# Kernel optimization log

Measured on AMD Instinct MI355X. Metric: run time of the kernel, lower is better.

Reference implementation:

```python
import jax, jax.numpy as jnp
import numpy as np


def setup_inputs() -> dict:
    key = jax.random.key(0)
    k1, k2, k3, k4 = jax.random.split(key, 4)
    B, C, Cr, H, W = 4, 32, 16, 64, 128
    return {
        "left_img": jax.random.normal(k1, (B, C, H, W), dtype=jnp.float32),
        "reduce_left_img": jax.random.normal(k2, (B, Cr, H, W), dtype=jnp.float32),
        "right_img": jax.random.normal(k3, (B, C, H, W), dtype=jnp.float32),
        "reduce_right_img": jax.random.normal(k4, (B, Cr, H, W), dtype=jnp.float32),
        "max_disp": 48,
    }


def reference(left_img, reduce_left_img, right_img, reduce_right_img, max_disp):
    # left_img, right_img: [B, C, H, W]; reduce_*: [B, Cr, H, W]
    B, C, H, W = left_img.shape
    D = int(max_disp)
    d = jnp.arange(D)
    cols = jnp.arange(W)
    # valid columns j >= disparity i, zero elsewhere (matches zero_() buffers)
    mask = (cols[None, :] >= d[:, None]).astype(left_img.dtype)  # [D, W]
    mask5 = mask[:, None, :]                                     # [D, 1, W] -> bcast [B,Ch,D,H,W]
    src = jnp.clip(cols[None, :] - d[:, None], 0, W - 1)         # [D, W] shifted source cols

    def shift(x):
        # x: [B, Ch, H, W] -> right-shifted by d with zero fill: [B, Ch, D, H, W]
        y = x[:, :, :, src]              # [B, Ch, H, D, W]
        return jnp.moveaxis(y, 3, 2) * mask5

    l = left_img[:, :, None, :, :] * mask5   # [B, C, D, H, W]
    r = shift(right_img)                     # [B, C, D, H, W]
    ave = (l + r) / 2
    ave2 = (l * l + r * r) / 2
    cost_var = ave2 - ave * ave              # = ((l-r)/2)^2, zero where masked

    cat_l = reduce_left_img[:, :, None, :, :] * mask5  # [B, Cr, D, H, W]
    cat_r = shift(reduce_right_img)                    # [B, Cr, D, H, W]

    # torch: cat((cost_var, cost_cat), 1) with cost_cat = [left_half, right_half]
    return jnp.concatenate([cost_var, cat_l, cat_r], axis=1)
```

## Files before the change

### kernel.cpp

```cpp
#include <hip/hip_runtime.h>

typedef unsigned int u32;
typedef float f32x4 __attribute__((ext_vector_type(4)));

__global__ __launch_bounds__(256) void costvol_kernel(
    const float* __restrict__ left, const float* __restrict__ rleft,
    const float* __restrict__ right, const float* __restrict__ rright,
    float* __restrict__ out)
{
    const u32 bid = blockIdx.x;
    const u32 h = bid & 63u;
    const u32 t = bid >> 6;
    const u32 c = t & 63u;
    const u32 b = t >> 6;
    const u32 tid = threadIdx.x;

    __shared__ float rrow[132];

    const u32 w0 = (tid & 31u) * 4u;
    const u32 d0 = tid >> 5;
    float* orow = out + (size_t)((b * 64u + c) * 48u) * 8192u
                      + (size_t)h * 128u + w0;

    if (c < 32u) {
        const u32 base = ((b * 32u + c) * 64u + h) * 128u;
        if (tid < 128u) rrow[tid + (tid >> 5)] = right[base + tid];
        __syncthreads();

        const float4 l = ((const float4*)(left + base))[tid & 31u];
        const float lv[4] = { l.x, l.y, l.z, l.w };

        #pragma unroll
        for (u32 it = 0; it < 6u; ++it) {
            const u32 d = it * 8u + d0;
            float o[4];
            #pragma unroll
            for (int j = 0; j < 4; ++j) {
                const u32 w = w0 + (u32)j;
                const bool act = (w >= d);
                const u32 idx = act ? (w - d) : 0u;
                const float r = rrow[idx + (idx >> 5)];
                const float tv = (lv[j] - r) * 0.5f;
                o[j] = act ? (tv * tv) : 0.0f;
            }
            f32x4 ov = { o[0], o[1], o[2], o[3] };
            __builtin_nontemporal_store(ov, (f32x4*)(orow + d * 8192u));
        }
    } else if (c < 48u) {
        const u32 base = ((b * 16u + (c - 32u)) * 64u + h) * 128u;
        const float4 v = ((const float4*)(rleft + base))[tid & 31u];

        #pragma unroll
        for (u32 it = 0; it < 6u; ++it) {
            const u32 d = it * 8u + d0;
            f32x4 ov = { (w0      >= d) ? v.x : 0.0f,
                         (w0 + 1u >= d) ? v.y : 0.0f,
                         (w0 + 2u >= d) ? v.z : 0.0f,
                         (w0 + 3u >= d) ? v.w : 0.0f };
            __builtin_nontemporal_store(ov, (f32x4*)(orow + d * 8192u));
        }
    } else {
        const u32 base = ((b * 16u + (c - 48u)) * 64u + h) * 128u;
        if (tid < 128u) rrow[tid + (tid >> 5)] = rright[base + tid];
        __syncthreads();

        #pragma unroll
        for (u32 it = 0; it < 6u; ++it) {
            const u32 d = it * 8u + d0;
            float o[4];
            #pragma unroll
            for (int j = 0; j < 4; ++j) {
                const u32 w = w0 + (u32)j;
                const bool act = (w >= d);
                const u32 idx = act ? (w - d) : 0u;
                o[j] = act ? rrow[idx + (idx >> 5)] : 0.0f;
            }
            f32x4 ov = { o[0], o[1], o[2], o[3] };
            __builtin_nontemporal_store(ov, (f32x4*)(orow + d * 8192u));
        }
    }
}

extern "C" void kernel_launch(void* const* d_in, const int* in_sizes, int n_in,
                              void* d_out, int out_size, void* d_ws, size_t ws_size,
                              hipStream_t stream) {
    const float* left   = (const float*)d_in[0];
    const float* rleft  = (const float*)d_in[1];
    const float* right  = (const float*)d_in[2];
    const float* rright = (const float*)d_in[3];
    float* out = (float*)d_out;
    const u32 blocks = 4u * 64u * 64u;
    costvol_kernel<<<blocks, 256, 0, stream>>>(left, rleft, right, rright, out);
}
```

Before: 393.8 us.

## Remap blocks to one output (b,c,d) plane with contiguous stores

```diff
diff --git a/kernel.cpp b/kernel.cpp
--- a/kernel.cpp
+++ b/kernel.cpp
@@ -9,74 +9,64 @@
     float* __restrict__ out)
 {
     const u32 bid = blockIdx.x;
-    const u32 h = bid & 63u;
-    const u32 t = bid >> 6;
+    const u32 d = bid % 48u;
+    const u32 t = bid / 48u;
     const u32 c = t & 63u;
     const u32 b = t >> 6;
     const u32 tid = threadIdx.x;
 
-    __shared__ float rrow[132];
-
-    const u32 w0 = (tid & 31u) * 4u;
-    const u32 d0 = tid >> 5;
-    float* orow = out + (size_t)((b * 64u + c) * 48u) * 8192u
-                      + (size_t)h * 128u + w0;
+    float* oplane = out + (size_t)bid * 8192u;
 
     if (c < 32u) {
-        const u32 base = ((b * 32u + c) * 64u + h) * 128u;
-        if (tid < 128u) rrow[tid + (tid >> 5)] = right[base + tid];
-        __syncthreads();
-
-        const float4 l = ((const float4*)(left + base))[tid & 31u];
-        const float lv[4] = { l.x, l.y, l.z, l.w };
-
+        const float* lp = left  + (size_t)(b * 32u + c) * 8192u;
+        const float* rp = right + (size_t)(b * 32u + c) * 8192u;
         #pragma unroll
-        for (u32 it = 0; it < 6u; ++it) {
-            const u32 d = it * 8u + d0;
+        for (u32 it = 0; it < 8u; ++it) {
+            const u32 flat = it * 1024u + tid * 4u;
+            const u32 w0 = flat & 127u;
+            const f32x4 l4 = *(const f32x4*)(lp + flat);
             float o[4];
             #pragma unroll
             for (int j = 0; j < 4; ++j) {
                 const u32 w = w0 + (u32)j;
                 const bool act = (w >= d);
-                const u32 idx = act ? (w - d) : 0u;
-                const float r = rrow[idx + (idx >> 5)];
-                const float tv = (lv[j] - r) * 0.5f;
+                const u32 ri = act ? (flat + (u32)j - d) : 0u;
+                const float r = rp[ri];
+                const float tv = (l4[j] - r) * 0.5f;
                 o[j] = act ? (tv * tv) : 0.0f;
             }
             f32x4 ov = { o[0], o[1], o[2], o[3] };
-            __builtin_nontemporal_store(ov, (f32x4*)(orow + d * 8192u));
+            __builtin_nontemporal_store(ov, (f32x4*)(oplane + flat));
         }
     } else if (c < 48u) {
-        const u32 base = ((b * 16u + (c - 32u)) * 64u + h) * 128u;
-        const float4 v = ((const float4*)(rleft + base))[tid & 31u];
-
+        const float* sp = rleft + (size_t)(b * 16u + (c - 32u)) * 8192u;
         #pragma unroll
-        for (u32 it = 0; it < 6u; ++it) {
-            const u32 d = it * 8u + d0;
-            f32x4 ov = { (w0      >= d) ? v.x : 0.0f,
-                         (w0 + 1u >= d) ? v.y : 0.0f,
-                         (w0 + 2u >= d) ? v.z : 0.0f,
-                         (w0 + 3u >= d) ? v.w : 0.0f };
-            __builtin_nontemporal_store(ov, (f32x4*)(orow + d * 8192u));
+        for (u32 it = 0; it < 8u; ++it) {
+            const u32 flat = it * 1024u + tid * 4u;
+            const u32 w0 = flat & 127u;
+            const f32x4 v = *(const f32x4*)(sp + flat);
+            f32x4 ov = { (w0      >= d) ? v[0] : 0.0f,
+                         (w0 + 1u >= d) ? v[1] : 0.0f,
+                         (w0 + 2u >= d) ? v[2] : 0.0f,
+                         (w0 + 3u >= d) ? v[3] : 0.0f };
+            __builtin_nontemporal_store(ov, (f32x4*)(oplane + flat));
         }
     } else {
-        const u32 base = ((b * 16u + (c - 48u)) * 64u + h) * 128u;
-        if (tid < 128u) rrow[tid + (tid >> 5)] = rright[base + tid];
-        __syncthreads();
-
+        const float* sp = rright + (size_t)(b * 16u + (c - 48u)) * 8192u;
         #pragma unroll
-        for (u32 it = 0; it < 6u; ++it) {
-            const u32 d = it * 8u + d0;
+        for (u32 it = 0; it < 8u; ++it) {
+            const u32 flat = it * 1024u + tid * 4u;
+            const u32 w0 = flat & 127u;
             float o[4];
             #pragma unroll
             for (int j = 0; j < 4; ++j) {
                 const u32 w = w0 + (u32)j;
                 const bool act = (w >= d);
-                const u32 idx = act ? (w - d) : 0u;
-                o[j] = act ? rrow[idx + (idx >> 5)] : 0.0f;
+                const u32 ri = act ? (flat + (u32)j - d) : 0u;
+                o[j] = act ? sp[ri] : 0.0f;
             }
             f32x4 ov = { o[0], o[1], o[2], o[3] };
-            __builtin_nontemporal_store(ov, (f32x4*)(orow + d * 8192u));
+            __builtin_nontemporal_store(ov, (f32x4*)(oplane + flat));
         }
     }
 }
@@ -89,6 +79,6 @@
     const float* right  = (const float*)d_in[2];
     const float* rright = (const float*)d_in[3];
     float* out = (float*)d_out;
-    const u32 blocks = 4u * 64u * 64u;
+    const u32 blocks = 4u * 64u * 48u;
     costvol_kernel<<<blocks, 256, 0, stream>>>(left, rleft, right, rright, out);
 }
```

New measurement: 452.1 us. +14.8%, slower.
